# Performance work log

Measured on AMD Instinct MI355X. Metric: run time of the kernel, lower is better.

Reference implementation:

```python
import jax, jax.numpy as jnp
import numpy as np

N_NODES = 100000


def gcn_conv(x, W, b, src, dst, norm, n_nodes):
    # x: [N, F_in] -> [N, F_out]; GCNConv: D^-1/2 (A+I) D^-1/2 (X W) + b
    h = x @ W                                   # [N, F_out]
    msg = h[src] * norm[:, None]                # [E+N, F_out] gather + scale
    out = jax.ops.segment_sum(msg, dst, num_segments=n_nodes)  # scatter-add
    return out + b


def setup_inputs() -> dict:
    key = jax.random.key(0)
    k0, k1, k2, k3, k4, k5 = jax.random.split(key, 6)
    n, e, f_in, f_hid, n_cls = N_NODES, 1600000, 128, 128, 3
    x = jax.random.normal(k0, (n, f_in), dtype=jnp.float32)
    edge_index = jax.random.randint(k1, (2, e), 0, n, dtype=jnp.int64)
    s1 = 1.0 / np.sqrt(f_in)
    s2 = 1.0 / np.sqrt(f_hid)
    W1 = jax.random.uniform(k2, (f_in, f_hid), jnp.float32, -s1, s1)
    b1 = jnp.zeros((f_hid,), jnp.float32)
    W2 = jax.random.uniform(k3, (f_hid, f_hid), jnp.float32, -s2, s2)
    b2 = jnp.zeros((f_hid,), jnp.float32)
    Wfc = jax.random.uniform(k4, (f_hid, n_cls), jnp.float32, -s2, s2)
    bfc = jax.random.uniform(k5, (n_cls,), jnp.float32, -s2, s2)
    return {"x": x, "edge_index": edge_index, "W1": W1, "b1": b1,
            "W2": W2, "b2": b2, "Wfc": Wfc, "bfc": bfc}


def reference(x, edge_index, W1, b1, W2, b2, Wfc, bfc):
    n = x.shape[0]
    # add self-loops (PyG GCNConv default add_self_loops=True)
    loops = jnp.arange(n, dtype=edge_index.dtype)
    src = jnp.concatenate([edge_index[0], loops])
    dst = jnp.concatenate([edge_index[1], loops])
    deg = jax.ops.segment_sum(jnp.ones_like(dst, dtype=x.dtype), dst,
                              num_segments=n)
    dinv = jax.lax.rsqrt(deg)                   # deg >= 1 due to self-loops
    norm = dinv[src] * dinv[dst]                # [E+N]
    h = jax.nn.relu(gcn_conv(x, W1, b1, src, dst, norm, n))   # dropout=eval id
    h = jax.nn.relu(gcn_conv(h, W2, b2, src, dst, norm, n))
    return jnp.tanh(h @ Wfc + bfc)              # [N, 3]
```

## Files before the change

kernel.cpp:

```cpp
#include <hip/hip_runtime.h>
#include <hip/hip_bf16.h>
#include <hip/hip_fp16.h>


#define NODE_F 128
#define NPLANE 8

typedef __attribute__((ext_vector_type(8))) short bf16x8;
typedef __attribute__((ext_vector_type(8))) unsigned short u16x8;
typedef __attribute__((ext_vector_type(4))) float f32x4;

__device__ inline unsigned short bf16_rn(float x) {
    unsigned u = __builtin_bit_cast(unsigned, x);
    unsigned r = (u + 0x7fffu + ((u >> 16) & 1u)) >> 16;
    return (unsigned short)r;
}
__device__ inline float bf16_to_f(unsigned short h) {
    unsigned u = (unsigned)h << 16;
    return __builtin_bit_cast(float, u);
}
__device__ inline void acc8_h(float a[8], uint4 v, float s) {
    unsigned vv[4] = {v.x, v.y, v.z, v.w};
    #pragma unroll
    for (int j = 0; j < 4; ++j) {
        float2 f = __half22float2(__builtin_bit_cast(__half2, vv[j]));
        a[2 * j]     += f.x * s;
        a[2 * j + 1] += f.y * s;
    }
}


__global__ __launch_bounds__(256) void wconv_kernel(const float* __restrict__ W1,
                                                    const float* __restrict__ W2,
                                                    unsigned short* __restrict__ WhiT,
                                                    unsigned short* __restrict__ WloT)
{
    const float* W = blockIdx.x ? W2 : W1;
    unsigned short* hiT = WhiT + blockIdx.x * 128 * 128;
    unsigned short* loT = WloT + blockIdx.x * 128 * 128;
    int tid = threadIdx.x;
    for (int i = tid; i < 128 * 128; i += 256) {
        int k = i >> 7, n = i & 127;
        float x = W[i];
        unsigned short hi = bf16_rn(x);
        float lo = x - bf16_to_f(hi);
        hiT[n * 128 + k] = hi;
        loT[n * 128 + k] = bf16_rn(lo);
    }
}


__global__ __launch_bounds__(256) void scan_block_kernel(
    int* __restrict__ degP, int* __restrict__ degTot,
    int* __restrict__ rsA, int* __restrict__ bsum, int N)
{
    __shared__ int s[256];
    const int tid = threadIdx.x;
    const int idx = blockIdx.x * 1024 + tid * 4;

    int tot[4];
    #pragma unroll
    for (int j4 = 0; j4 < 4; ++j4) {
        int node = idx + j4;
        int t = 0;
        if (node < N) {
            #pragma unroll
            for (int p = 0; p < NPLANE; ++p) {
                int v = degP[(size_t)p * N + node];
                degP[(size_t)p * N + node] = t;
                t += v;
            }
            degTot[node] = t;
        }
        tot[j4] = (node < N) ? t : 0;
    }

    int t = tot[0] + tot[1] + tot[2] + tot[3];
    s[tid] = t;
    __syncthreads();
    #pragma unroll
    for (int off = 1; off < 256; off <<= 1) {
        int x = (tid >= off) ? s[tid - off] : 0;
        __syncthreads();
        s[tid] += x;
        __syncthreads();
    }
    int excl = s[tid] - t;
    if (idx + 0 < N) rsA[idx + 0] = excl;
    if (idx + 1 < N) rsA[idx + 1] = excl + tot[0];
    if (idx + 2 < N) rsA[idx + 2] = excl + tot[0] + tot[1];
    if (idx + 3 < N) rsA[idx + 3] = excl + tot[0] + tot[1] + tot[2];
    if (tid == 255) bsum[blockIdx.x] = s[255];
}

__global__ __launch_bounds__(1024) void scan_tops_kernel(int* __restrict__ bsum, int nb) {
    __shared__ int s[1024];
    const int tid = threadIdx.x;
    int v = (tid < nb) ? bsum[tid] : 0;
    s[tid] = v;
    __syncthreads();
    #pragma unroll
    for (int off = 1; off < 1024; off <<= 1) {
        int x = (tid >= off) ? s[tid - off] : 0;
        __syncthreads();
        s[tid] += x;
        __syncthreads();
    }
    if (tid < nb) bsum[tid] = s[tid] - v;
}


__global__ __launch_bounds__(256) void finish_fill_kernel(
    const int* __restrict__ src, const int* __restrict__ dst,
    const unsigned short* __restrict__ rank,
    const int* __restrict__ rsA, const int* __restrict__ bsum,
    const int* __restrict__ degP, const int* __restrict__ degTot,
    int* __restrict__ rsB, float* __restrict__ dinv,
    int* __restrict__ csr_src, int E, int N, int fill_blocks)
{
    if ((int)blockIdx.x < fill_blocks) {
        int e = blockIdx.x * 256 + threadIdx.x;
        if (e < E) {
            int d = dst[e];
            int p = e & (NPLANE - 1);
            csr_src[rsA[d] + bsum[d >> 10] + degP[(size_t)p * N + d] + (int)rank[e]] = src[e];
        }
    } else {
        int i = (blockIdx.x - fill_blocks) * 256 + threadIdx.x;
        if (i < N) {
            int rs = rsA[i] + bsum[i >> 10];
            rsB[i] = rs;
            dinv[i] = rsqrtf((float)degTot[i] + 1.0f);
            if (i == N - 1) rsB[N] = rs + degTot[i];
        }
    }
}


template<bool SCALE_OUT>
__device__ __forceinline__ void gemm_compute(
    const unsigned short* __restrict__ WhiT, const unsigned short* __restrict__ WloT,
    const float* __restrict__ dinv, __half* __restrict__ Hout, int N, int rbase,
    unsigned short* xhi, unsigned short* xlo)
{
    const int tid  = threadIdx.x;
    const int lane = tid & 63;
    const int w    = tid >> 6;

    bf16x8 bhi[2][4], blo[2][4];
    {
        int n0   = w * 32 + (lane & 15);
        int koct = (lane >> 4) * 8;
        #pragma unroll
        for (int nt = 0; nt < 2; ++nt) {
            #pragma unroll
            for (int kk = 0; kk < 4; ++kk) {
                size_t o = (size_t)(n0 + nt * 16) * 128 + kk * 32 + koct;
                bhi[nt][kk] = *reinterpret_cast<const bf16x8*>(WhiT + o);
                blo[nt][kk] = *reinterpret_cast<const bf16x8*>(WloT + o);
            }
        }
    }

    f32x4 acc[4][2];
    #pragma unroll
    for (int m = 0; m < 4; ++m)
        #pragma unroll
        for (int nt = 0; nt < 2; ++nt)
            acc[m][nt] = (f32x4){0.f, 0.f, 0.f, 0.f};

    #pragma unroll
    for (int kk = 0; kk < 4; ++kk) {
        #pragma unroll
        for (int m = 0; m < 4; ++m) {
            int row  = m * 16 + (lane & 15);
            int koff = kk * 64 + (lane >> 4) * 16;
            int byte = row * 256 + (koff ^ ((row & 7) << 4));
            bf16x8 ahi = *reinterpret_cast<const bf16x8*>(reinterpret_cast<char*>(xhi) + byte);
            bf16x8 alo = *reinterpret_cast<const bf16x8*>(reinterpret_cast<char*>(xlo) + byte);
            #pragma unroll
            for (int nt = 0; nt < 2; ++nt) {
                acc[m][nt] = __builtin_amdgcn_mfma_f32_16x16x32_bf16(ahi, bhi[nt][kk], acc[m][nt], 0, 0, 0);
                acc[m][nt] = __builtin_amdgcn_mfma_f32_16x16x32_bf16(ahi, blo[nt][kk], acc[m][nt], 0, 0, 0);
                acc[m][nt] = __builtin_amdgcn_mfma_f32_16x16x32_bf16(alo, bhi[nt][kk], acc[m][nt], 0, 0, 0);
            }
        }
    }

    #pragma unroll
    for (int m = 0; m < 4; ++m) {
        int row = rbase + m * 16 + (lane >> 4) * 4;
        int col = w * 32 + (lane & 15);
        #pragma unroll
        for (int nt = 0; nt < 2; ++nt) {
            #pragma unroll
            for (int r = 0; r < 4; ++r) {
                if (row + r < N) {
                    float v = acc[m][nt][r];
                    if (SCALE_OUT) v *= dinv[row + r];
                    Hout[(size_t)(row + r) * NODE_F + col + nt * 16] = __float2half(v);
                }
            }
        }
    }
}


__device__ __forceinline__ void gemm1_body(
    const float* __restrict__ Xf,
    const unsigned short* __restrict__ WhiT, const unsigned short* __restrict__ WloT,
    __half* __restrict__ Hout, int N, int bid,
    unsigned short* xhi, unsigned short* xlo)
{
    const int tid   = threadIdx.x;
    const int rbase = bid * 64;

    #pragma unroll
    for (int it = 0; it < 8; ++it) {
        int f   = it * 256 + tid;
        int row = f >> 5;
        int k4  = f & 31;
        float4 v = make_float4(0.f, 0.f, 0.f, 0.f);
        if (rbase + row < N)
            v = *reinterpret_cast<const float4*>(Xf + (size_t)(rbase + row) * NODE_F + k4 * 4);
        float xs[4] = {v.x, v.y, v.z, v.w};
        ushort4 h4, l4;
        unsigned short* hp = &h4.x;
        unsigned short* lp = &l4.x;
        #pragma unroll
        for (int j = 0; j < 4; ++j) {
            unsigned short hi = bf16_rn(xs[j]);
            hp[j] = hi;
            lp[j] = bf16_rn(xs[j] - bf16_to_f(hi));
        }
        int byte = row * 256 + ((k4 * 8) ^ ((row & 7) << 4));
        *reinterpret_cast<ushort4*>(reinterpret_cast<char*>(xhi) + byte) = h4;
        *reinterpret_cast<ushort4*>(reinterpret_cast<char*>(xlo) + byte) = l4;
    }
    __syncthreads();
    gemm_compute<false>(WhiT, WloT, nullptr, Hout, N, rbase, xhi, xlo);
}


__global__ __launch_bounds__(256) void gemm1deg_kernel(
    const int* __restrict__ dst, int* __restrict__ degP,
    unsigned short* __restrict__ rank, int E,
    int edge_blocks, int gemm_blocks,
    const float* __restrict__ X, const unsigned short* __restrict__ WhiT,
    const unsigned short* __restrict__ WloT, __half* __restrict__ H, int N)
{
    __shared__ unsigned short xhi[64 * 128];
    __shared__ unsigned short xlo[64 * 128];
    int q = blockIdx.x / 5, r = blockIdx.x % 5;
    if (r == 4) {
        int stride = edge_blocks * 256;
        for (int e = q * 256 + threadIdx.x; e < E; e += stride) {
            int p = e & (NPLANE - 1);
            rank[e] = (unsigned short)atomicAdd(&degP[(size_t)p * N + dst[e]], 1);
        }
    } else {
        int gid = q * 4 + r;
        if (gid < gemm_blocks)
            gemm1_body(X, WhiT, WloT, H, N, gid, xhi, xlo);
    }
}


template<bool EDGE_SCALE>
__device__ __forceinline__ void gather_core(
    const __half* __restrict__ Hs, const int* __restrict__ csr_src,
    const int* __restrict__ row_start, const float* __restrict__ dinv,
    int node, int ql, int qi, float a[8])
{
    const char* Hb = reinterpret_cast<const char*>(Hs);
    #pragma unroll
    for (int j = 0; j < 8; ++j) a[j] = 0.f;
    if (qi == 0) {
        float ds = EDGE_SCALE ? dinv[node] : 1.0f;
        acc8_h(a, *reinterpret_cast<const uint4*>(Hb + ((size_t)node * 256 + ql * 16)), ds);
    }

    int i   = row_start[node];
    int end = row_start[node + 1];
    for (; i + 15 < end; i += 16) {
        int s0 = csr_src[i + qi];
        int s1 = csr_src[i + 4 + qi];
        int s2 = csr_src[i + 8 + qi];
        int s3 = csr_src[i + 12 + qi];
        float d0 = EDGE_SCALE ? dinv[s0] : 1.0f;
        float d1 = EDGE_SCALE ? dinv[s1] : 1.0f;
        float d2 = EDGE_SCALE ? dinv[s2] : 1.0f;
        float d3 = EDGE_SCALE ? dinv[s3] : 1.0f;
        uint4 v0 = *reinterpret_cast<const uint4*>(Hb + ((size_t)s0 * 256 + ql * 16));
        uint4 v1 = *reinterpret_cast<const uint4*>(Hb + ((size_t)s1 * 256 + ql * 16));
        uint4 v2 = *reinterpret_cast<const uint4*>(Hb + ((size_t)s2 * 256 + ql * 16));
        uint4 v3 = *reinterpret_cast<const uint4*>(Hb + ((size_t)s3 * 256 + ql * 16));
        acc8_h(a, v0, d0);
        acc8_h(a, v1, d1);
        acc8_h(a, v2, d2);
        acc8_h(a, v3, d3);
    }
    for (; i + 7 < end; i += 8) {
        int s0 = csr_src[i + qi];
        int s1 = csr_src[i + 4 + qi];
        float d0 = EDGE_SCALE ? dinv[s0] : 1.0f;
        float d1 = EDGE_SCALE ? dinv[s1] : 1.0f;
        uint4 v0 = *reinterpret_cast<const uint4*>(Hb + ((size_t)s0 * 256 + ql * 16));
        uint4 v1 = *reinterpret_cast<const uint4*>(Hb + ((size_t)s1 * 256 + ql * 16));
        acc8_h(a, v0, d0);
        acc8_h(a, v1, d1);
    }
    for (; i < end; i += 4) {
        if (i + qi < end) {
            int s = csr_src[i + qi];
            float ds = EDGE_SCALE ? dinv[s] : 1.0f;
            acc8_h(a, *reinterpret_cast<const uint4*>(Hb + ((size_t)s * 256 + ql * 16)), ds);
        }
    }
    #pragma unroll
    for (int j = 0; j < 8; ++j) {
        a[j] += __shfl_xor(a[j], 32);
        a[j] += __shfl_xor(a[j], 16);
    }
}


__global__ __launch_bounds__(256) void gather1_kernel(
    const __half* __restrict__ H, const int* __restrict__ csr_src,
    const int* __restrict__ row_start, const float* __restrict__ dinv,
    const float* __restrict__ b, __half* __restrict__ A1, int N)
{
    int node = (blockIdx.x * blockDim.x + threadIdx.x) >> 6;
    int lane = threadIdx.x & 63;
    int ql = lane & 15, qi = lane >> 4;
    if (node >= N) return;

    float a[8];
    gather_core<true>(H, csr_src, row_start, dinv, node, ql, qi, a);

    if (qi == 0) {
        const float dd = dinv[node];
        u16x8 o;
        #pragma unroll
        for (int j = 0; j < 8; ++j) {
            float r = fmaxf(b[ql * 8 + j] + dd * a[j], 0.f);
            o[j] = __builtin_bit_cast(unsigned short, __float2half(r));
        }
        *reinterpret_cast<u16x8*>(reinterpret_cast<char*>(A1) + ((size_t)node * 256 + ql * 16)) = o;
    }
}


__global__ __launch_bounds__(256) void gemm2_kernel(
    const __half* __restrict__ A1,
    const unsigned short* __restrict__ WhiT, const unsigned short* __restrict__ WloT,
    const float* __restrict__ dinv, __half* __restrict__ Hs, int N)
{
    __shared__ unsigned short xhi[64 * 128];
    __shared__ unsigned short xlo[64 * 128];
    const int tid   = threadIdx.x;
    const int rbase = blockIdx.x * 64;

    #pragma unroll
    for (int it = 0; it < 4; ++it) {
        int idx = it * 256 + tid;
        int row = idx >> 4;
        int k8  = idx & 15;
        u16x8 h = {0, 0, 0, 0, 0, 0, 0, 0};
        u16x8 l = {0, 0, 0, 0, 0, 0, 0, 0};
        if (rbase + row < N) {
            u16x8 v = *reinterpret_cast<const u16x8*>(
                reinterpret_cast<const char*>(A1) + ((size_t)(rbase + row) * 256 + k8 * 16));
            #pragma unroll
            for (int j = 0; j < 8; ++j) {
                float f = __half2float(__builtin_bit_cast(__half, (unsigned short)v[j]));
                unsigned short hi = bf16_rn(f);
                h[j] = hi;
                l[j] = bf16_rn(f - bf16_to_f(hi));
            }
        }
        int byte = row * 256 + ((k8 * 16) ^ ((row & 7) << 4));
        *reinterpret_cast<u16x8*>(reinterpret_cast<char*>(xhi) + byte) = h;
        *reinterpret_cast<u16x8*>(reinterpret_cast<char*>(xlo) + byte) = l;
    }
    __syncthreads();
    gemm_compute<true>(WhiT, WloT, dinv, Hs, N, rbase, xhi, xlo);
}


__global__ __launch_bounds__(256) void gather2fc_kernel(
    const __half* __restrict__ Hs, const int* __restrict__ csr_src,
    const int* __restrict__ row_start, const float* __restrict__ dinv,
    const float* __restrict__ b, const float* __restrict__ Wfc,
    const float* __restrict__ bfc, float* __restrict__ out, int N)
{
    int node = (blockIdx.x * blockDim.x + threadIdx.x) >> 6;
    int lane = threadIdx.x & 63;
    int ql = lane & 15, qi = lane >> 4;
    if (node >= N) return;

    float a[8];
    gather_core<false>(Hs, csr_src, row_start, dinv, node, ql, qi, a);

    const float dd = dinv[node];
    float p0 = 0.f, p1 = 0.f, p2 = 0.f;
    #pragma unroll
    for (int j = 0; j < 8; ++j) {
        float r = fmaxf(b[ql * 8 + j] + dd * a[j], 0.f);
        const float* wr = Wfc + (size_t)(ql * 8 + j) * 3;
        p0 += r * wr[0]; p1 += r * wr[1]; p2 += r * wr[2];
    }
    #pragma unroll
    for (int off = 8; off > 0; off >>= 1) {
        p0 += __shfl_down(p0, off);
        p1 += __shfl_down(p1, off);
        p2 += __shfl_down(p2, off);
    }
    if (lane == 0) {
        out[(size_t)node * 3 + 0] = tanhf(p0 + bfc[0]);
        out[(size_t)node * 3 + 1] = tanhf(p1 + bfc[1]);
        out[(size_t)node * 3 + 2] = tanhf(p2 + bfc[2]);
    }
}

extern "C" void kernel_launch(void* const* d_in, const int* in_sizes, int n_in,
                              void* d_out, int out_size, void* d_ws, size_t ws_size,
                              hipStream_t stream)
{
    const float* x    = (const float*)d_in[0];
    const int*   edge = (const int*)d_in[1];
    const float* W1   = (const float*)d_in[2];
    const float* b1   = (const float*)d_in[3];
    const float* W2   = (const float*)d_in[4];
    const float* b2   = (const float*)d_in[5];
    const float* Wfc  = (const float*)d_in[6];
    const float* bfc  = (const float*)d_in[7];
    float* out = (float*)d_out;

    const int N = in_sizes[0] / NODE_F;
    const int E = in_sizes[1] / 2;
    const int* src = edge;
    const int* dst = edge + E;

    char* ws = (char*)d_ws;
    size_t off = 0;
    auto alloc = [&](size_t bytes) {
        void* p = ws + off;
        off += (bytes + 511) & ~511ull;
        return p;
    };
    const int nblk = (N + 1023) / 1024;
    float* dinv      = (float*)alloc((size_t)N * 4);
    int*   degP      = (int*)  alloc((size_t)NPLANE * N * 4);
    int*   degTot    = (int*)  alloc((size_t)N * 4);
    unsigned short* rank = (unsigned short*)alloc((size_t)E * 2);
    int*   rsA       = (int*)  alloc((size_t)N * 4);
    int*   rsB       = (int*)  alloc((size_t)(N + 1) * 4);
    int*   bsum      = (int*)  alloc((size_t)nblk * 4);
    int*   csr_src   = (int*)  alloc((size_t)E * 4);
    unsigned short* WhiT = (unsigned short*)alloc(2 * 128 * 128 * 2);
    unsigned short* WloT = (unsigned short*)alloc(2 * 128 * 128 * 2);
    __half* H        = (__half*)alloc((size_t)N * NODE_F * 2);
    __half* A1       = (__half*)alloc((size_t)N * NODE_F * 2);
    __half* H2       = (__half*)alloc((size_t)N * NODE_F * 2);
    (void)ws_size; (void)n_in; (void)out_size;

    const int B = 256;
    const int gemm_grid   = (N + 63) / 64;
    const int gather_grid = (N + 3) / 4;
    const int fill_blocks = (E + B - 1) / B;
    const int fin_blocks  = (N + B - 1) / B;

    const int edge_blocks  = (gemm_grid + 3) / 4;
    const int total_blocks = gemm_grid + edge_blocks + 4;

    wconv_kernel<<<2, B, 0, stream>>>(W1, W2, WhiT, WloT);
    hipMemsetAsync(degP, 0, (size_t)NPLANE * N * 4, stream);

    gemm1deg_kernel<<<total_blocks, B, 0, stream>>>(
        dst, degP, rank, E, edge_blocks, gemm_grid, x, WhiT, WloT, H, N);

    scan_block_kernel<<<nblk, B, 0, stream>>>(degP, degTot, rsA, bsum, N);
    scan_tops_kernel<<<1, 1024, 0, stream>>>(bsum, nblk);

    finish_fill_kernel<<<fill_blocks + fin_blocks, B, 0, stream>>>(
        src, dst, rank, rsA, bsum, degP, degTot, rsB, dinv, csr_src, E, N, fill_blocks);

    gather1_kernel<<<gather_grid, B, 0, stream>>>(H, csr_src, rsB, dinv, b1, A1, N);

    gemm2_kernel<<<gemm_grid, B, 0, stream>>>(A1, WhiT + 128 * 128, WloT + 128 * 128,
                                              dinv, H2, N);

    gather2fc_kernel<<<gather_grid, B, 0, stream>>>(H2, csr_src, rsB, dinv, b2,
                                                    Wfc, bfc, out, N);
}
```

Before: 311.9 us.

## Prescale H by source dinv before gather1 and accumulate with fdot2

Instead of loading dinv[src] per edge in the first gather, the layer-1 features are prescaled in place by each row's inverse sqrt degree, using extra blocks appended to the finish/fill kernel. The gather core then needs no per-edge scale. It accumulates fp16 pairs straight into fp32 with the fdot2 intrinsic against one-hot half vectors, which replaces the convert-then-multiply sequence. This drops a random per-edge dinv load and some ALU work, but adds a full read-modify-write pass over H and an extra fp16 rounding of the scaled values.

```diff
diff --git a/kernel.cpp b/kernel.cpp
--- a/kernel.cpp
+++ b/kernel.cpp
@@ -9,6 +9,7 @@
 typedef __attribute__((ext_vector_type(8))) short bf16x8;
 typedef __attribute__((ext_vector_type(8))) unsigned short u16x8;
 typedef __attribute__((ext_vector_type(4))) float f32x4;
+typedef _Float16 h2v __attribute__((ext_vector_type(2)));
 
 __device__ inline unsigned short bf16_rn(float x) {
     unsigned u = __builtin_bit_cast(unsigned, x);
@@ -19,13 +20,16 @@
     unsigned u = (unsigned)h << 16;
     return __builtin_bit_cast(float, u);
 }
-__device__ inline void acc8_h(float a[8], uint4 v, float s) {
+
+__device__ inline void acc8_d(float a[8], uint4 v) {
+    const h2v e0 = __builtin_bit_cast(h2v, (unsigned)0x00003C00);
+    const h2v e1 = __builtin_bit_cast(h2v, (unsigned)0x3C000000);
     unsigned vv[4] = {v.x, v.y, v.z, v.w};
     #pragma unroll
     for (int j = 0; j < 4; ++j) {
-        float2 f = __half22float2(__builtin_bit_cast(__half2, vv[j]));
-        a[2 * j]     += f.x * s;
-        a[2 * j + 1] += f.y * s;
+        h2v h = __builtin_bit_cast(h2v, vv[j]);
+        a[2 * j]     = __builtin_amdgcn_fdot2(h, e0, a[2 * j],     false);
+        a[2 * j + 1] = __builtin_amdgcn_fdot2(h, e1, a[2 * j + 1], false);
     }
 }
 
@@ -116,7 +120,8 @@
     const int* __restrict__ rsA, const int* __restrict__ bsum,
     const int* __restrict__ degP, const int* __restrict__ degTot,
     int* __restrict__ rsB, float* __restrict__ dinv,
-    int* __restrict__ csr_src, int E, int N, int fill_blocks)
+    int* __restrict__ csr_src, __half* __restrict__ H,
+    int E, int N, int fill_blocks, int fin_blocks)
 {
     if ((int)blockIdx.x < fill_blocks) {
         int e = blockIdx.x * 256 + threadIdx.x;
@@ -125,13 +130,26 @@
             int p = e & (NPLANE - 1);
             csr_src[rsA[d] + bsum[d >> 10] + degP[(size_t)p * N + d] + (int)rank[e]] = src[e];
         }
-    } else {
+    } else if ((int)blockIdx.x < fill_blocks + fin_blocks) {
         int i = (blockIdx.x - fill_blocks) * 256 + threadIdx.x;
         if (i < N) {
             int rs = rsA[i] + bsum[i >> 10];
             rsB[i] = rs;
             dinv[i] = rsqrtf((float)degTot[i] + 1.0f);
             if (i == N - 1) rsB[N] = rs + degTot[i];
+        }
+    } else {
+        int idx = (blockIdx.x - fill_blocks - fin_blocks) * 256 + threadIdx.x;
+        if (idx < N * 16) {
+            int row = idx >> 4;
+            float ds = rsqrtf((float)degTot[row] + 1.0f);
+            __half2* p = reinterpret_cast<__half2*>(H) + (size_t)idx * 4;
+            #pragma unroll
+            for (int j = 0; j < 4; ++j) {
+                float2 v = __half22float2(p[j]);
+                v.x *= ds; v.y *= ds;
+                p[j] = __float22half2_rn(v);
+            }
         }
     }
 }
@@ -266,19 +284,15 @@
 }
 
 
-template<bool EDGE_SCALE>
 __device__ __forceinline__ void gather_core(
     const __half* __restrict__ Hs, const int* __restrict__ csr_src,
-    const int* __restrict__ row_start, const float* __restrict__ dinv,
-    int node, int ql, int qi, float a[8])
+    const int* __restrict__ row_start, int node, int ql, int qi, float a[8])
 {
     const char* Hb = reinterpret_cast<const char*>(Hs);
     #pragma unroll
     for (int j = 0; j < 8; ++j) a[j] = 0.f;
-    if (qi == 0) {
-        float ds = EDGE_SCALE ? dinv[node] : 1.0f;
-        acc8_h(a, *reinterpret_cast<const uint4*>(Hb + ((size_t)node * 256 + ql * 16)), ds);
-    }
+    if (qi == 0)
+        acc8_d(a, *reinterpret_cast<const uint4*>(Hb + ((size_t)node * 256 + ql * 16)));
 
     int i   = row_start[node];
     int end = row_start[node + 1];
@@ -287,34 +301,27 @@
         int s1 = csr_src[i + 4 + qi];
         int s2 = csr_src[i + 8 + qi];
         int s3 = csr_src[i + 12 + qi];
-        float d0 = EDGE_SCALE ? dinv[s0] : 1.0f;
-        float d1 = EDGE_SCALE ? dinv[s1] : 1.0f;
-        float d2 = EDGE_SCALE ? dinv[s2] : 1.0f;
-        float d3 = EDGE_SCALE ? dinv[s3] : 1.0f;
         uint4 v0 = *reinterpret_cast<const uint4*>(Hb + ((size_t)s0 * 256 + ql * 16));
         uint4 v1 = *reinterpret_cast<const uint4*>(Hb + ((size_t)s1 * 256 + ql * 16));
         uint4 v2 = *reinterpret_cast<const uint4*>(Hb + ((size_t)s2 * 256 + ql * 16));
         uint4 v3 = *reinterpret_cast<const uint4*>(Hb + ((size_t)s3 * 256 + ql * 16));
-        acc8_h(a, v0, d0);
-        acc8_h(a, v1, d1);
-        acc8_h(a, v2, d2);
-        acc8_h(a, v3, d3);
+        acc8_d(a, v0);
+        acc8_d(a, v1);
+        acc8_d(a, v2);
+        acc8_d(a, v3);
     }
     for (; i + 7 < end; i += 8) {
         int s0 = csr_src[i + qi];
         int s1 = csr_src[i + 4 + qi];
-        float d0 = EDGE_SCALE ? dinv[s0] : 1.0f;
-        float d1 = EDGE_SCALE ? dinv[s1] : 1.0f;
         uint4 v0 = *reinterpret_cast<const uint4*>(Hb + ((size_t)s0 * 256 + ql * 16));
         uint4 v1 = *reinterpret_cast<const uint4*>(Hb + ((size_t)s1 * 256 + ql * 16));
-        acc8_h(a, v0, d0);
-        acc8_h(a, v1, d1);
+        acc8_d(a, v0);
+        acc8_d(a, v1);
     }
     for (; i < end; i += 4) {
         if (i + qi < end) {
             int s = csr_src[i + qi];
-            float ds = EDGE_SCALE ? dinv[s] : 1.0f;
-            acc8_h(a, *reinterpret_cast<const uint4*>(Hb + ((size_t)s * 256 + ql * 16)), ds);
+            acc8_d(a, *reinterpret_cast<const uint4*>(Hb + ((size_t)s * 256 + ql * 16)));
         }
     }
     #pragma unroll
@@ -326,7 +333,7 @@
 
 
 __global__ __launch_bounds__(256) void gather1_kernel(
-    const __half* __restrict__ H, const int* __restrict__ csr_src,
+    const __half* __restrict__ Hs, const int* __restrict__ csr_src,
     const int* __restrict__ row_start, const float* __restrict__ dinv,
     const float* __restrict__ b, __half* __restrict__ A1, int N)
 {
@@ -336,7 +343,7 @@
     if (node >= N) return;
 
     float a[8];
-    gather_core<true>(H, csr_src, row_start, dinv, node, ql, qi, a);
+    gather_core(Hs, csr_src, row_start, node, ql, qi, a);
 
     if (qi == 0) {
         const float dd = dinv[node];
@@ -400,7 +407,7 @@
     if (node >= N) return;
 
     float a[8];
-    gather_core<false>(Hs, csr_src, row_start, dinv, node, ql, qi, a);
+    gather_core(Hs, csr_src, row_start, node, ql, qi, a);
 
     const float dd = dinv[node];
     float p0 = 0.f, p1 = 0.f, p2 = 0.f;
@@ -470,6 +477,7 @@
     const int gather_grid = (N + 3) / 4;
     const int fill_blocks = (E + B - 1) / B;
     const int fin_blocks  = (N + B - 1) / B;
+    const int scale_blocks = (N * 16 + B - 1) / B;
 
     const int edge_blocks  = (gemm_grid + 3) / 4;
     const int total_blocks = gemm_grid + edge_blocks + 4;
@@ -483,8 +491,9 @@
     scan_block_kernel<<<nblk, B, 0, stream>>>(degP, degTot, rsA, bsum, N);
     scan_tops_kernel<<<1, 1024, 0, stream>>>(bsum, nblk);
 
-    finish_fill_kernel<<<fill_blocks + fin_blocks, B, 0, stream>>>(
-        src, dst, rank, rsA, bsum, degP, degTot, rsB, dinv, csr_src, E, N, fill_blocks);
+    finish_fill_kernel<<<fill_blocks + fin_blocks + scale_blocks, B, 0, stream>>>(
+        src, dst, rank, rsA, bsum, degP, degTot, rsB, dinv, csr_src, H,
+        E, N, fill_blocks, fin_blocks);
 
     gather1_kernel<<<gather_grid, B, 0, stream>>>(H, csr_src, rsB, dinv, b1, A1, N);
 
```

Measured after the change: 317.8 us. Within noise of the previous version (+1.9%).
